# Optimization experiments

Measured on AMD Instinct MI355X. Metric: run time of the kernel, lower is better.

## Reference

```python
import jax, jax.numpy as jnp
import numpy as np

B, S, D, H, O, E, K = 4, 1024, 1024, 2048, 1024, 8, 2
LOAD_BALANCE_WEIGHT = 0.01


def setup_inputs() -> dict:
    key = jax.random.key(0)
    ks = jax.random.split(key, 9)
    scale = 0.02
    return {
        "x": jax.random.normal(ks[0], (B, S, D), jnp.float32),
        "Wg": scale * jax.random.normal(ks[1], (D, E), jnp.float32),
        "bg": jnp.zeros((E,), jnp.float32),
        "W1": scale * jax.random.normal(ks[2], (E, D, H), jnp.float32),
        "b1": jnp.zeros((E, H), jnp.float32),
        "W2": scale * jax.random.normal(ks[3], (E, H, H), jnp.float32),
        "b2": jnp.zeros((E, H), jnp.float32),
        "W3": scale * jax.random.normal(ks[4], (E, H, O), jnp.float32),
        "b3": jnp.zeros((E, O), jnp.float32),
    }


def reference(x, Wg, bg, W1, b1, W2, b2, W3, b3):
    # Eval-mode MoE: no gating noise, dropout is identity.
    b, s, d = x.shape
    e = Wg.shape[1]

    # --- gating: noisy top-k gating (noise off in eval) ---
    raw_gates = x @ Wg + bg                         # [B,S,E]
    topk_logits, topk_idx = jax.lax.top_k(raw_gates, K)  # [B,S,K]
    gates = jax.nn.softmax(topk_logits, axis=-1)    # [B,S,K]

    # Combine weights per expert: scatter top-k gates into [B,S,E].
    onehot = jax.nn.one_hot(topk_idx, e, dtype=x.dtype)      # [B,S,K,E]
    combine = jnp.sum(onehot * gates[..., None], axis=-2)    # [B,S,E]

    # --- expert MLPs (dense grouped GEMM over all tokens) ---
    xt = x.reshape(-1, d)            # [T,D]
    wt = combine.reshape(-1, e)      # [T,E]
    h = jax.nn.relu(jnp.einsum('td,edh->eth', xt, W1) + b1[:, None, :])
    h = jax.nn.relu(jnp.einsum('eth,ehg->etg', h, W2) + b2[:, None, :])
    y = jnp.einsum('eth,eho->eto', h, W3) + b3[:, None, :]   # [E,T,O]
    out = jnp.einsum('te,eto->to', wt, y).reshape(b, s, -1)  # [B,S,O]

    # --- auxiliary losses ---
    gate_probs = jax.nn.softmax(raw_gates, axis=-1)          # [B,S,E]
    avg_gate_probs = gate_probs.mean(axis=(0, 1))            # [E]
    avg_expert_counts = combine.mean(axis=(0, 1))            # [E]
    load_balance_loss = LOAD_BALANCE_WEIGHT * e * jnp.sum(avg_gate_probs * avg_expert_counts)
    gate_entropy = -jnp.sum(avg_gate_probs * jnp.log(avg_gate_probs + 1e-8))

    return out, load_balance_loss, avg_expert_counts, gate_entropy
```

## Files before the change

### kernel.cpp

```cpp
#include <hip/hip_runtime.h>
#include <hip/hip_bf16.h>
#include <math.h>

#define T_TOK 4096
#define D_IN  1024
#define H_DIM 2048
#define O_DIM 1024
#define NE    8
#define ROWCAP 9216
#define RT128  72

typedef __bf16 bf16x8 __attribute__((ext_vector_type(8)));
typedef __bf16 bf16x4 __attribute__((ext_vector_type(4)));
typedef float  f32x4  __attribute__((ext_vector_type(4)));

#define ELT(f, j) ((j) == 0 ? (f).x : (j) == 1 ? (f).y : (j) == 2 ? (f).z : (f).w)

__device__ __forceinline__ void gl_lds16(const void* g, void* l) {
    __builtin_amdgcn_global_load_lds(
        (const __attribute__((address_space(1))) void*)g,
        (__attribute__((address_space(3))) void*)l, 16, 0, 0);
}

__global__ __launch_bounds__(256) void gating_kernel(
    const float* __restrict__ x, const float* __restrict__ Wg, const float* __restrict__ bg,
    __bf16* __restrict__ xb, float* __restrict__ gates_tk, int* __restrict__ idx_tk,
    int* __restrict__ cnt_part, double* __restrict__ prob_part, double* __restrict__ gsum_part)
{
    __shared__ float WgS[8][1032];
    __shared__ float bgS[NE];
    __shared__ double tok_p[32][NE];
    __shared__ double tok_g[32][2];
    __shared__ int    tok_i[32][2];
    const int tid = threadIdx.x;

    for (int i = tid; i < D_IN * NE; i += 256)
        WgS[i >> 10][i & 1023] = Wg[i];
    if (tid < NE) bgS[tid] = bg[tid];

    {
        const size_t base = (size_t)blockIdx.x * 32 * D_IN;
        for (int i = tid * 4; i < 32 * D_IN; i += 256 * 4) {
            float4 v = *(const float4*)(x + base + i);
            bf16x4 b = {(__bf16)v.x, (__bf16)v.y, (__bf16)v.z, (__bf16)v.w};
            *(bf16x4*)(xb + base + i) = b;
        }
    }
    __syncthreads();

    const int tokL = tid >> 3;
    const int part = tid & 7;
    const int t = blockIdx.x * 32 + tokL;
    const float* xr = x + (size_t)t * D_IN + part * 128;

    double s[NE] = {0, 0, 0, 0, 0, 0, 0, 0};
    for (int j = 0; j < 128; j += 4) {
        float4 xv = *(const float4*)(xr + j);
        const float* w = &WgS[part][j * 8];
        #pragma unroll
        for (int jj = 0; jj < 4; ++jj) {
            double xd = (double)(ELT(xv, jj));
            #pragma unroll
            for (int e = 0; e < NE; ++e)
                s[e] += xd * (double)w[jj * 8 + e];
        }
    }
    #pragma unroll
    for (int off = 4; off; off >>= 1)
        #pragma unroll
        for (int e = 0; e < NE; ++e)
            s[e] += __shfl_xor(s[e], off);

    if (part == 0) {
        double rg[NE];
        #pragma unroll
        for (int e = 0; e < NE; ++e) rg[e] = s[e] + (double)bgS[e];
        int i0 = 0;
        #pragma unroll
        for (int e = 1; e < NE; ++e) if (rg[e] > rg[i0]) i0 = e;
        int i1 = -1;
        #pragma unroll
        for (int e = 0; e < NE; ++e) {
            if (e == i0) continue;
            if (i1 < 0 || rg[e] > rg[i1]) i1 = e;
        }
        double e1 = exp(rg[i1] - rg[i0]);
        double den = 1.0 + e1;
        gates_tk[t * 2] = (float)(1.0 / den); gates_tk[t * 2 + 1] = (float)(e1 / den);
        idx_tk[t * 2] = i0;   idx_tk[t * 2 + 1] = i1;
        tok_g[tokL][0] = 1.0 / den; tok_g[tokL][1] = e1 / den;
        tok_i[tokL][0] = i0;        tok_i[tokL][1] = i1;
        double mx = rg[0];
        #pragma unroll
        for (int e = 1; e < NE; ++e) mx = fmax(mx, rg[e]);
        double pe[NE], sum = 0.0;
        #pragma unroll
        for (int e = 0; e < NE; ++e) { pe[e] = exp(rg[e] - mx); sum += pe[e]; }
        #pragma unroll
        for (int e = 0; e < NE; ++e) tok_p[tokL][e] = pe[e] / sum;
    }
    __syncthreads();
    if (tid < NE) {
        double p = 0.0, g = 0.0; int c = 0;
        for (int i = 0; i < 32; ++i) {
            p += tok_p[i][tid];
            if (tok_i[i][0] == tid) { g += tok_g[i][0]; ++c; }
            if (tok_i[i][1] == tid) { g += tok_g[i][1]; ++c; }
        }
        prob_part[blockIdx.x * NE + tid] = p;
        gsum_part[blockIdx.x * NE + tid] = g;
        cnt_part[blockIdx.x * NE + tid] = c;
    }
}

__global__ __launch_bounds__(256) void route_tokens(
    const int* __restrict__ cnt_part, const int* __restrict__ idx_tk,
    int* __restrict__ poffset, int* __restrict__ totalp,
    int* __restrict__ token_ids, int* __restrict__ t2r)
{
    __shared__ int cntE[NE], baseE[NE];
    __shared__ int po[NE + 1];
    __shared__ int4 sb[256];
    const int tid = threadIdx.x;
    const int b = blockIdx.x;

    if (tid < NE) {
        int tot = 0, pre = 0;
        for (int g = 0; g < 128; ++g) {
            int v = cnt_part[g * NE + tid];
            tot += v;
            if (g < b * 8) pre += v;
        }
        cntE[tid] = tot;
        baseE[tid] = pre;
    }
    __syncthreads();
    if (tid == 0) {
        po[0] = 0;
        for (int e = 0; e < NE; ++e) po[e + 1] = po[e] + ((cntE[e] + 127) & ~127);
        if (b == 0) {
            for (int e = 0; e <= NE; ++e) poffset[e] = po[e];
            totalp[0] = po[NE];
        }
    }
    __syncthreads();

    const int t = b * 256 + tid;
    const int e0 = idx_tk[t * 2], e1 = idx_tk[t * 2 + 1];
    int4 p = {0, 0, 0, 0};
    ((int*)&p)[e0 >> 1] += 1 << ((e0 & 1) * 16);
    ((int*)&p)[e1 >> 1] += 1 << ((e1 & 1) * 16);
    sb[tid] = p;
    __syncthreads();
    for (int off = 1; off < 256; off <<= 1) {
        int4 v = sb[tid];
        int4 u = {0, 0, 0, 0};
        if (tid >= off) u = sb[tid - off];
        __syncthreads();
        v.x += u.x; v.y += u.y; v.z += u.z; v.w += u.w;
        sb[tid] = v;
        __syncthreads();
    }
    int4 inc = sb[tid];
    {
        int pos0 = ((((const int*)&inc)[e0 >> 1] >> ((e0 & 1) * 16)) & 0xffff) - 1;
        int r0 = po[e0] + baseE[e0] + pos0;
        token_ids[r0] = t; t2r[t * 2] = r0;
        int pos1 = ((((const int*)&inc)[e1 >> 1] >> ((e1 & 1) * 16)) & 0xffff) - 1;
        int r1 = po[e1] + baseE[e1] + pos1;
        token_ids[r1] = t; t2r[t * 2 + 1] = r1;
    }
    for (int e = 0; e < NE; ++e) {
        int c = cntE[e], base = po[e], pc = po[e + 1] - po[e];
        for (int i = c + b * 256 + tid; i < pc; i += 16 * 256) token_ids[base + i] = 0;
    }
}

template<bool GATHER, bool RELU, bool OUTBF16>
__global__ __launch_bounds__(256) void gemm_expert(
    const __bf16* __restrict__ A, int lda,
    const float* __restrict__ Bw, int Kdim, int N,
    const float* __restrict__ bias,
    void* __restrict__ Out, int ldo,
    const int* __restrict__ token_ids,
    const int* __restrict__ poffset,
    const int* __restrict__ totalp)
{
    __shared__ __bf16 As[128 * 64];
    __shared__ __bf16 Bs[128 * 64];
    const int tid = threadIdx.x;
    const int row0 = blockIdx.y * 128;
    if (row0 >= totalp[0]) return;
    int e = 0;
    while (e < NE - 1 && row0 >= poffset[e + 1]) ++e;
    const int n0 = blockIdx.x * 128;
    const float* Be = Bw + (size_t)e * Kdim * N;
    const float* biase = bias + (size_t)e * N;

    const int srow = tid >> 3;
    const int jperm = (tid & 7) ^ (srow & 7);
    const int scol = jperm * 8;
    int arow_g[4];
    #pragma unroll
    for (int c = 0; c < 4; ++c) {
        int r = row0 + c * 32 + srow;
        arow_g[c] = GATHER ? token_ids[r] : r;
    }

    const int rg = tid >> 5;
    const int cB = tid & 31;
    const float* bsrc0 = Be + (size_t)rg * 8 * N + n0 + cB * 4;

    const int lane = tid & 63;
    const int quad = lane >> 4;
    const int m16  = lane & 15;
    const int wave = tid >> 6;
    const int wm = wave >> 1, wn = wave & 1;

    f32x4 acc[4][4];
    #pragma unroll
    for (int i = 0; i < 4; ++i)
        #pragma unroll
        for (int j = 0; j < 4; ++j)
            acc[i][j] = (f32x4){0.f, 0.f, 0.f, 0.f};

    const int niter = Kdim >> 6;

    float4 r[8];
    #pragma unroll
    for (int i = 0; i < 8; ++i)
        r[i] = *(const float4*)(bsrc0 + (size_t)i * N);

    for (int kt = 0; kt < niter; ++kt) {
        const int kofs = kt * 64 + scol;
        #pragma unroll
        for (int c = 0; c < 4; ++c)
            gl_lds16(A + (size_t)arow_g[c] * lda + kofs, (char*)As + c * 4096 + tid * 16);
        #pragma unroll
        for (int j = 0; j < 4; ++j) {
            const int n = cB * 4 + j;
            const int key = (n & 7) ^ ((n >> 4) & 3);
            bf16x8 v;
            #pragma unroll
            for (int i = 0; i < 8; ++i) v[i] = (__bf16)(ELT(r[i], j));
            *(bf16x8*)&Bs[n * 64 + ((rg ^ key) << 3)] = v;
        }
        __syncthreads();
        if (kt + 1 < niter) {
            const float* bsrc = bsrc0 + (size_t)(kt + 1) * 64 * N;
            #pragma unroll
            for (int i = 0; i < 8; ++i)
                r[i] = *(const float4*)(bsrc + (size_t)i * N);
        }
        #pragma unroll
        for (int ks = 0; ks < 2; ++ks) {
            const int c0 = (ks << 2) | quad;
            const int pA = c0 ^ (m16 & 7);
            bf16x8 af[4], bfr[4];
            #pragma unroll
            for (int i = 0; i < 4; ++i)
                af[i] = *(const bf16x8*)&As[(wm * 64 + i * 16 + m16) * 64 + pA * 8];
            #pragma unroll
            for (int j = 0; j < 4; ++j) {
                const int pB = pA ^ j;
                bfr[j] = *(const bf16x8*)&Bs[(wn * 64 + j * 16 + m16) * 64 + pB * 8];
            }
            #pragma unroll
            for (int i = 0; i < 4; ++i)
                #pragma unroll
                for (int j = 0; j < 4; ++j)
                    acc[i][j] = __builtin_amdgcn_mfma_f32_16x16x32_bf16(af[i], bfr[j], acc[i][j], 0, 0, 0);
        }
        __syncthreads();
    }
    #pragma unroll
    for (int i = 0; i < 4; ++i)
        #pragma unroll
        for (int j = 0; j < 4; ++j)
            #pragma unroll
            for (int rr = 0; rr < 4; ++rr) {
                int grow = row0 + wm * 64 + i * 16 + quad * 4 + rr;
                int gcol = n0 + wn * 64 + j * 16 + m16;
                float v = acc[i][j][rr] + biase[gcol];
                if (RELU) v = v > 0.f ? v : 0.f;
                if (OUTBF16) ((__bf16*)Out)[(size_t)grow * ldo + gcol] = (__bf16)v;
                else         ((float*)Out)[(size_t)grow * ldo + gcol] = v;
            }
}

__global__ __launch_bounds__(256) void combine_out(
    const float* __restrict__ y, const float* __restrict__ gates_tk,
    const int* __restrict__ t2r, float* __restrict__ out,
    const double* __restrict__ prob_part, const double* __restrict__ gsum_part)
{
    const int t = blockIdx.x;
    const int o = threadIdx.x * 4;
    const int r0 = t2r[t * 2], r1 = t2r[t * 2 + 1];
    const float g0 = gates_tk[t * 2], g1 = gates_tk[t * 2 + 1];
    float4 a = *(const float4*)&y[(size_t)r0 * O_DIM + o];
    float4 b = *(const float4*)&y[(size_t)r1 * O_DIM + o];
    float4 c;
    c.x = g0 * a.x + g1 * b.x;
    c.y = g0 * a.y + g1 * b.y;
    c.z = g0 * a.z + g1 * b.z;
    c.w = g0 * a.w + g1 * b.w;
    *(float4*)&out[(size_t)t * O_DIM + o] = c;

    if (blockIdx.x == 0) {
        __shared__ double ps[NE], gs[NE];
        const int tid = threadIdx.x;
        if (tid < NE) {
            double p = 0.0, g = 0.0;
            for (int bb = 0; bb < 128; ++bb) {
                p += prob_part[bb * NE + tid];
                g += gsum_part[bb * NE + tid];
            }
            ps[tid] = p / (double)T_TOK;
            gs[tid] = g / (double)T_TOK;
            out[(size_t)T_TOK * O_DIM + 1 + tid] = (float)(g / (double)T_TOK);
        }
        __syncthreads();
        if (tid == 0) {
            double lb = 0.0, ent = 0.0;
            for (int e = 0; e < NE; ++e) {
                lb += ps[e] * gs[e];
                ent -= ps[e] * log(ps[e] + 1e-8);
            }
            out[(size_t)T_TOK * O_DIM] = (float)(0.01 * 8.0 * lb);
            out[(size_t)T_TOK * O_DIM + 9] = (float)ent;
        }
    }
}

extern "C" void kernel_launch(void* const* d_in, const int* in_sizes, int n_in,
                              void* d_out, int out_size, void* d_ws, size_t ws_size,
                              hipStream_t stream)
{
    const float* x  = (const float*)d_in[0];
    const float* Wg = (const float*)d_in[1];
    const float* bg = (const float*)d_in[2];
    const float* W1 = (const float*)d_in[3];
    const float* b1 = (const float*)d_in[4];
    const float* W2 = (const float*)d_in[5];
    const float* b2 = (const float*)d_in[6];
    const float* W3 = (const float*)d_in[7];
    const float* b3 = (const float*)d_in[8];
    float* out = (float*)d_out;
    char* ws = (char*)d_ws;

    size_t off = 0;
    __bf16* xb  = (__bf16*)(ws + off); off += (size_t)T_TOK * D_IN * 2;
    __bf16* h1  = (__bf16*)(ws + off);
    float*  y   = (float*) (ws + off); off += (size_t)ROWCAP * H_DIM * 2;
    __bf16* h2  = (__bf16*)(ws + off); off += (size_t)ROWCAP * H_DIM * 2;
    float* gates_tk = (float*)(ws + off); off += T_TOK * 2 * 4;
    int* idx_tk     = (int*)(ws + off);   off += T_TOK * 2 * 4;
    int* t2r        = (int*)(ws + off);   off += T_TOK * 2 * 4;
    int* token_ids  = (int*)(ws + off);   off += ROWCAP * 4;
    double* prob_part = (double*)(ws + off); off += 128 * NE * 8;
    double* gsum_part = (double*)(ws + off); off += 128 * NE * 8;
    int* cnt_part   = (int*)(ws + off);   off += 128 * NE * 4;
    int* poffset    = (int*)(ws + off);   off += (NE + 1) * 4;
    int* totalp     = (int*)(ws + off);   off += 16;

    gating_kernel<<<128, 256, 0, stream>>>(x, Wg, bg, xb, gates_tk, idx_tk,
                                           cnt_part, prob_part, gsum_part);
    route_tokens<<<16, 256, 0, stream>>>(cnt_part, idx_tk, poffset, totalp, token_ids, t2r);
    gemm_expert<true,  true,  true ><<<dim3(H_DIM / 128, RT128), 256, 0, stream>>>(
        xb, D_IN, W1, D_IN, H_DIM, b1, (void*)h1, H_DIM, token_ids, poffset, totalp);
    gemm_expert<false, true,  true ><<<dim3(H_DIM / 128, RT128), 256, 0, stream>>>(
        h1, H_DIM, W2, H_DIM, H_DIM, b2, (void*)h2, H_DIM, token_ids, poffset, totalp);
    gemm_expert<false, false, false><<<dim3(O_DIM / 128, RT128), 256, 0, stream>>>(
        h2, H_DIM, W3, H_DIM, O_DIM, b3, (void*)y, O_DIM, token_ids, poffset, totalp);
    combine_out<<<T_TOK, 256, 0, stream>>>(y, gates_tk, t2r, out, prob_part, gsum_part);
}
```

Before: 574.2 us.

## Fuse MoE pipeline into persistent megakernel with grid barriers and bf16 weight pre-conversion

Replaces the six separate launches with one persistent kernel of 512 blocks. Phases are separated by an atomic grid barrier, and GEMM tiles are spread across blocks in a strided loop. While the gating blocks run, the other blocks convert W1/W2/W3 from fp32 to bf16 in workspace, so the GEMMs load half-width weights and skip per-tile conversion. This trades launch gaps and repeated fp32 weight traffic for a full weight conversion pass every call and barrier overhead. It also relies on all 512 blocks being co-resident, and the barrier's bounded spin could silently break ordering.

Result: slower. 1.757 ms (+205.9%).

```diff
diff --git a/kernel.cpp b/kernel.cpp
--- a/kernel.cpp
+++ b/kernel.cpp
@@ -8,7 +8,8 @@
 #define O_DIM 1024
 #define NE    8
 #define ROWCAP 9216
-#define RT128  72
+#define NBLK  512
+#define GBLK  128
 
 typedef __bf16 bf16x8 __attribute__((ext_vector_type(8)));
 typedef __bf16 bf16x4 __attribute__((ext_vector_type(4)));
@@ -22,41 +23,82 @@
         (__attribute__((address_space(3))) void*)l, 16, 0, 0);
 }
 
-__global__ __launch_bounds__(256) void gating_kernel(
-    const float* __restrict__ x, const float* __restrict__ Wg, const float* __restrict__ bg,
-    __bf16* __restrict__ xb, float* __restrict__ gates_tk, int* __restrict__ idx_tk,
-    int* __restrict__ cnt_part, double* __restrict__ prob_part, double* __restrict__ gsum_part)
-{
-    __shared__ float WgS[8][1032];
-    __shared__ float bgS[NE];
-    __shared__ double tok_p[32][NE];
-    __shared__ double tok_g[32][2];
-    __shared__ int    tok_i[32][2];
-    const int tid = threadIdx.x;
-
+struct MoeArgs {
+    const float *x, *Wg, *bg, *W1, *b1, *W2, *b2, *W3, *b3;
+    float* out;
+    __bf16 *xb, *h1, *h2;
+    float* y;
+    __bf16 *W1b, *W2b, *W3b;
+    float* gates_tk;
+    int *idx_tk, *t2r, *token_ids;
+    double *prob_part, *gsum_part;
+    int *cnt_part, *poffset, *totalp;
+    int *bar;
+};
+
+__device__ __forceinline__ void grid_barrier(int* bar, int phase)
+{
+    __syncthreads();
+    __threadfence();
+    if (threadIdx.x == 0) {
+        __hip_atomic_fetch_add(bar, 1, __ATOMIC_RELEASE, __HIP_MEMORY_SCOPE_AGENT);
+        const int target = phase * NBLK;
+        int spins = 0;
+        while (__hip_atomic_load(bar, __ATOMIC_ACQUIRE, __HIP_MEMORY_SCOPE_AGENT) < target) {
+            __builtin_amdgcn_s_sleep(2);
+            if (++spins > (1 << 20)) break;
+        }
+    }
+    __syncthreads();
+    __threadfence();
+}
+
+union SharedU {
+    struct {
+        float WgS[8][1032];
+        float bgS[NE];
+        double tok_p[32][NE];
+        double tok_g[32][2];
+        int    tok_i[32][2];
+    } g;
+    struct {
+        int cntE[NE], baseE[NE], po[NE + 1];
+        int4 sb[256];
+    } r;
+    struct {
+        __bf16 As[128 * 64];
+        __bf16 Bs[128 * 64];
+    } m;
+    struct {
+        double ps[NE], gs[NE];
+    } f;
+};
+
+__device__ void gating_body(const int b, const int tid, const MoeArgs& a, SharedU& sh)
+{
     for (int i = tid; i < D_IN * NE; i += 256)
-        WgS[i >> 10][i & 1023] = Wg[i];
-    if (tid < NE) bgS[tid] = bg[tid];
+        sh.g.WgS[i >> 10][i & 1023] = a.Wg[i];
+    if (tid < NE) sh.g.bgS[tid] = a.bg[tid];
 
     {
-        const size_t base = (size_t)blockIdx.x * 32 * D_IN;
+        const size_t base = (size_t)b * 32 * D_IN;
         for (int i = tid * 4; i < 32 * D_IN; i += 256 * 4) {
-            float4 v = *(const float4*)(x + base + i);
-            bf16x4 b = {(__bf16)v.x, (__bf16)v.y, (__bf16)v.z, (__bf16)v.w};
-            *(bf16x4*)(xb + base + i) = b;
+            float4 v = *(const float4*)(a.x + base + i);
+            bf16x4 bv = {(__bf16)v.x, (__bf16)v.y, (__bf16)v.z, (__bf16)v.w};
+            *(bf16x4*)(a.xb + base + i) = bv;
         }
     }
     __syncthreads();
 
     const int tokL = tid >> 3;
     const int part = tid & 7;
-    const int t = blockIdx.x * 32 + tokL;
-    const float* xr = x + (size_t)t * D_IN + part * 128;
+    const int t = b * 32 + tokL;
+    const float* xr = a.x + (size_t)t * D_IN + part * 128;
 
     double s[NE] = {0, 0, 0, 0, 0, 0, 0, 0};
     for (int j = 0; j < 128; j += 4) {
         float4 xv = *(const float4*)(xr + j);
-        const float* w = &WgS[part][j * 8];
+        const float* w = &sh.g.WgS[part][j * 8];
         #pragma unroll
         for (int jj = 0; jj < 4; ++jj) {
             double xd = (double)(ELT(xv, jj));
@@ -74,7 +116,7 @@
     if (part == 0) {
         double rg[NE];
         #pragma unroll
-        for (int e = 0; e < NE; ++e) rg[e] = s[e] + (double)bgS[e];
+        for (int e = 0; e < NE; ++e) rg[e] = s[e] + (double)sh.g.bgS[e];
         int i0 = 0;
         #pragma unroll
         for (int e = 1; e < NE; ++e) if (rg[e] > rg[i0]) i0 = e;
@@ -86,10 +128,10 @@
         }
         double e1 = exp(rg[i1] - rg[i0]);
         double den = 1.0 + e1;
-        gates_tk[t * 2] = (float)(1.0 / den); gates_tk[t * 2 + 1] = (float)(e1 / den);
-        idx_tk[t * 2] = i0;   idx_tk[t * 2 + 1] = i1;
-        tok_g[tokL][0] = 1.0 / den; tok_g[tokL][1] = e1 / den;
-        tok_i[tokL][0] = i0;        tok_i[tokL][1] = i1;
+        a.gates_tk[t * 2] = (float)(1.0 / den); a.gates_tk[t * 2 + 1] = (float)(e1 / den);
+        a.idx_tk[t * 2] = i0;   a.idx_tk[t * 2 + 1] = i1;
+        sh.g.tok_g[tokL][0] = 1.0 / den; sh.g.tok_g[tokL][1] = e1 / den;
+        sh.g.tok_i[tokL][0] = i0;        sh.g.tok_i[tokL][1] = i1;
         double mx = rg[0];
         #pragma unroll
         for (int e = 1; e < NE; ++e) mx = fmax(mx, rg[e]);
@@ -97,37 +139,51 @@
         #pragma unroll
         for (int e = 0; e < NE; ++e) { pe[e] = exp(rg[e] - mx); sum += pe[e]; }
         #pragma unroll
-        for (int e = 0; e < NE; ++e) tok_p[tokL][e] = pe[e] / sum;
+        for (int e = 0; e < NE; ++e) sh.g.tok_p[tokL][e] = pe[e] / sum;
     }
     __syncthreads();
     if (tid < NE) {
         double p = 0.0, g = 0.0; int c = 0;
         for (int i = 0; i < 32; ++i) {
-            p += tok_p[i][tid];
-            if (tok_i[i][0] == tid) { g += tok_g[i][0]; ++c; }
-            if (tok_i[i][1] == tid) { g += tok_g[i][1]; ++c; }
-        }
-        prob_part[blockIdx.x * NE + tid] = p;
-        gsum_part[blockIdx.x * NE + tid] = g;
-        cnt_part[blockIdx.x * NE + tid] = c;
-    }
-}
-
-__global__ __launch_bounds__(256) void route_tokens(
-    const int* __restrict__ cnt_part, const int* __restrict__ idx_tk,
-    int* __restrict__ poffset, int* __restrict__ totalp,
-    int* __restrict__ token_ids, int* __restrict__ t2r)
-{
-    __shared__ int cntE[NE], baseE[NE];
-    __shared__ int po[NE + 1];
-    __shared__ int4 sb[256];
-    const int tid = threadIdx.x;
-    const int b = blockIdx.x;
+            p += sh.g.tok_p[i][tid];
+            if (sh.g.tok_i[i][0] == tid) { g += sh.g.tok_g[i][0]; ++c; }
+            if (sh.g.tok_i[i][1] == tid) { g += sh.g.tok_g[i][1]; ++c; }
+        }
+        a.prob_part[b * NE + tid] = p;
+        a.gsum_part[b * NE + tid] = g;
+        a.cnt_part[b * NE + tid] = c;
+    }
+}
+
+__device__ __forceinline__ void cvt_range(const float* __restrict__ src, __bf16* __restrict__ dst,
+                                          size_t n8, size_t start, size_t stride)
+{
+    for (size_t i = start; i < n8; i += stride) {
+        float4 va = ((const float4*)src)[2 * i];
+        float4 vb = ((const float4*)src)[2 * i + 1];
+        bf16x8 v = {(__bf16)va.x, (__bf16)va.y, (__bf16)va.z, (__bf16)va.w,
+                    (__bf16)vb.x, (__bf16)vb.y, (__bf16)vb.z, (__bf16)vb.w};
+        *(bf16x8*)(dst + i * 8) = v;
+    }
+}
+
+__device__ void cvt_body(const int cb, const int tid, const MoeArgs& a)
+{
+    const size_t start = (size_t)cb * 256 + tid;
+    const size_t stride = (size_t)(NBLK - GBLK) * 256;
+    cvt_range(a.W1, a.W1b, (size_t)NE * D_IN * H_DIM / 8, start, stride);
+    cvt_range(a.W2, a.W2b, (size_t)NE * H_DIM * H_DIM / 8, start, stride);
+    cvt_range(a.W3, a.W3b, (size_t)NE * H_DIM * O_DIM / 8, start, stride);
+}
+
+__device__ void route_body(const int b, const int tid, const MoeArgs& a, SharedU& sh)
+{
+    int* cntE = sh.r.cntE; int* baseE = sh.r.baseE; int* po = sh.r.po; int4* sb = sh.r.sb;
 
     if (tid < NE) {
         int tot = 0, pre = 0;
         for (int g = 0; g < 128; ++g) {
-            int v = cnt_part[g * NE + tid];
+            int v = a.cnt_part[g * NE + tid];
             tot += v;
             if (g < b * 8) pre += v;
         }
@@ -139,14 +195,14 @@
         po[0] = 0;
         for (int e = 0; e < NE; ++e) po[e + 1] = po[e] + ((cntE[e] + 127) & ~127);
         if (b == 0) {
-            for (int e = 0; e <= NE; ++e) poffset[e] = po[e];
-            totalp[0] = po[NE];
+            for (int e = 0; e <= NE; ++e) a.poffset[e] = po[e];
+            a.totalp[0] = po[NE];
         }
     }
     __syncthreads();
 
     const int t = b * 256 + tid;
-    const int e0 = idx_tk[t * 2], e1 = idx_tk[t * 2 + 1];
+    const int e0 = a.idx_tk[t * 2], e1 = a.idx_tk[t * 2 + 1];
     int4 p = {0, 0, 0, 0};
     ((int*)&p)[e0 >> 1] += 1 << ((e0 & 1) * 16);
     ((int*)&p)[e1 >> 1] += 1 << ((e1 & 1) * 16);
@@ -165,36 +221,32 @@
     {
         int pos0 = ((((const int*)&inc)[e0 >> 1] >> ((e0 & 1) * 16)) & 0xffff) - 1;
         int r0 = po[e0] + baseE[e0] + pos0;
-        token_ids[r0] = t; t2r[t * 2] = r0;
+        a.token_ids[r0] = t; a.t2r[t * 2] = r0;
         int pos1 = ((((const int*)&inc)[e1 >> 1] >> ((e1 & 1) * 16)) & 0xffff) - 1;
         int r1 = po[e1] + baseE[e1] + pos1;
-        token_ids[r1] = t; t2r[t * 2 + 1] = r1;
+        a.token_ids[r1] = t; a.t2r[t * 2 + 1] = r1;
     }
     for (int e = 0; e < NE; ++e) {
         int c = cntE[e], base = po[e], pc = po[e + 1] - po[e];
-        for (int i = c + b * 256 + tid; i < pc; i += 16 * 256) token_ids[base + i] = 0;
+        for (int i = c + b * 256 + tid; i < pc; i += 16 * 256) a.token_ids[base + i] = 0;
     }
 }
 
 template<bool GATHER, bool RELU, bool OUTBF16>
-__global__ __launch_bounds__(256) void gemm_expert(
+__device__ __forceinline__ void gemm_tile(
+    SharedU& sh, const int tid, const int n0, const int row0,
     const __bf16* __restrict__ A, int lda,
-    const float* __restrict__ Bw, int Kdim, int N,
+    const __bf16* __restrict__ Bw, int Kdim, int N,
     const float* __restrict__ bias,
     void* __restrict__ Out, int ldo,
     const int* __restrict__ token_ids,
-    const int* __restrict__ poffset,
-    const int* __restrict__ totalp)
-{
-    __shared__ __bf16 As[128 * 64];
-    __shared__ __bf16 Bs[128 * 64];
-    const int tid = threadIdx.x;
-    const int row0 = blockIdx.y * 128;
-    if (row0 >= totalp[0]) return;
+    const int* __restrict__ poffset)
+{
+    __bf16* As = sh.m.As;
+    __bf16* Bs = sh.m.Bs;
     int e = 0;
     while (e < NE - 1 && row0 >= poffset[e + 1]) ++e;
-    const int n0 = blockIdx.x * 128;
-    const float* Be = Bw + (size_t)e * Kdim * N;
+    const __bf16* Be = Bw + (size_t)e * Kdim * N;
     const float* biase = bias + (size_t)e * N;
 
     const int srow = tid >> 3;
@@ -209,7 +261,7 @@
 
     const int rg = tid >> 5;
     const int cB = tid & 31;
-    const float* bsrc0 = Be + (size_t)rg * 8 * N + n0 + cB * 4;
+    const __bf16* bsrc0 = Be + (size_t)rg * 8 * N + n0 + cB * 4;
 
     const int lane = tid & 63;
     const int quad = lane >> 4;
@@ -226,10 +278,10 @@
 
     const int niter = Kdim >> 6;
 
-    float4 r[8];
+    bf16x4 r[8];
     #pragma unroll
     for (int i = 0; i < 8; ++i)
-        r[i] = *(const float4*)(bsrc0 + (size_t)i * N);
+        r[i] = *(const bf16x4*)(bsrc0 + (size_t)i * N);
 
     for (int kt = 0; kt < niter; ++kt) {
         const int kofs = kt * 64 + scol;
@@ -242,15 +294,15 @@
             const int key = (n & 7) ^ ((n >> 4) & 3);
             bf16x8 v;
             #pragma unroll
-            for (int i = 0; i < 8; ++i) v[i] = (__bf16)(ELT(r[i], j));
+            for (int i = 0; i < 8; ++i) v[i] = r[i][j];
             *(bf16x8*)&Bs[n * 64 + ((rg ^ key) << 3)] = v;
         }
         __syncthreads();
         if (kt + 1 < niter) {
-            const float* bsrc = bsrc0 + (size_t)(kt + 1) * 64 * N;
+            const __bf16* bsrc = bsrc0 + (size_t)(kt + 1) * 64 * N;
             #pragma unroll
             for (int i = 0; i < 8; ++i)
-                r[i] = *(const float4*)(bsrc + (size_t)i * N);
+                r[i] = *(const bf16x4*)(bsrc + (size_t)i * N);
         }
         #pragma unroll
         for (int ks = 0; ks < 2; ++ks) {
@@ -288,71 +340,101 @@
             }
 }
 
-__global__ __launch_bounds__(256) void combine_out(
-    const float* __restrict__ y, const float* __restrict__ gates_tk,
-    const int* __restrict__ t2r, float* __restrict__ out,
-    const double* __restrict__ prob_part, const double* __restrict__ gsum_part)
-{
-    const int t = blockIdx.x;
-    const int o = threadIdx.x * 4;
-    const int r0 = t2r[t * 2], r1 = t2r[t * 2 + 1];
-    const float g0 = gates_tk[t * 2], g1 = gates_tk[t * 2 + 1];
-    float4 a = *(const float4*)&y[(size_t)r0 * O_DIM + o];
-    float4 b = *(const float4*)&y[(size_t)r1 * O_DIM + o];
-    float4 c;
-    c.x = g0 * a.x + g1 * b.x;
-    c.y = g0 * a.y + g1 * b.y;
-    c.z = g0 * a.z + g1 * b.z;
-    c.w = g0 * a.w + g1 * b.w;
-    *(float4*)&out[(size_t)t * O_DIM + o] = c;
-
-    if (blockIdx.x == 0) {
-        __shared__ double ps[NE], gs[NE];
-        const int tid = threadIdx.x;
+template<bool GATHER, bool RELU, bool OUTBF16>
+__device__ void gemm_phase(
+    SharedU& sh, const int bid, const int tid, const MoeArgs& a,
+    const __bf16* A, int lda, const __bf16* Bw, int Kdim, int N,
+    const float* bias, void* Out, int ldo)
+{
+    const int rtiles = (a.totalp[0] + 127) >> 7;
+    const int nx = N >> 7;
+    const int ntiles = nx * rtiles;
+    for (int tile = bid; tile < ntiles; tile += NBLK) {
+        const int n0 = (tile % nx) * 128;
+        const int row0 = (tile / nx) * 128;
+        gemm_tile<GATHER, RELU, OUTBF16>(sh, tid, n0, row0, A, lda, Bw, Kdim, N,
+                                         bias, Out, ldo, a.token_ids, a.poffset);
+    }
+}
+
+__device__ void combine_body(const int bid, const int tid, const MoeArgs& a, SharedU& sh)
+{
+    if (bid == 0) {
         if (tid < NE) {
             double p = 0.0, g = 0.0;
             for (int bb = 0; bb < 128; ++bb) {
-                p += prob_part[bb * NE + tid];
-                g += gsum_part[bb * NE + tid];
+                p += a.prob_part[bb * NE + tid];
+                g += a.gsum_part[bb * NE + tid];
             }
-            ps[tid] = p / (double)T_TOK;
-            gs[tid] = g / (double)T_TOK;
-            out[(size_t)T_TOK * O_DIM + 1 + tid] = (float)(g / (double)T_TOK);
+            sh.f.ps[tid] = p / (double)T_TOK;
+            sh.f.gs[tid] = g / (double)T_TOK;
+            a.out[(size_t)T_TOK * O_DIM + 1 + tid] = (float)(g / (double)T_TOK);
         }
         __syncthreads();
         if (tid == 0) {
             double lb = 0.0, ent = 0.0;
             for (int e = 0; e < NE; ++e) {
-                lb += ps[e] * gs[e];
-                ent -= ps[e] * log(ps[e] + 1e-8);
+                lb += sh.f.ps[e] * sh.f.gs[e];
+                ent -= sh.f.ps[e] * log(sh.f.ps[e] + 1e-8);
             }
-            out[(size_t)T_TOK * O_DIM] = (float)(0.01 * 8.0 * lb);
-            out[(size_t)T_TOK * O_DIM + 9] = (float)ent;
-        }
-    }
+            a.out[(size_t)T_TOK * O_DIM] = (float)(0.01 * 8.0 * lb);
+            a.out[(size_t)T_TOK * O_DIM + 9] = (float)ent;
+        }
+    }
+    const int o = tid * 4;
+    for (int t = bid; t < T_TOK; t += NBLK) {
+        const int r0 = a.t2r[t * 2], r1 = a.t2r[t * 2 + 1];
+        const float g0 = a.gates_tk[t * 2], g1 = a.gates_tk[t * 2 + 1];
+        float4 va = *(const float4*)&a.y[(size_t)r0 * O_DIM + o];
+        float4 vb = *(const float4*)&a.y[(size_t)r1 * O_DIM + o];
+        float4 c;
+        c.x = g0 * va.x + g1 * vb.x;
+        c.y = g0 * va.y + g1 * vb.y;
+        c.z = g0 * va.z + g1 * vb.z;
+        c.w = g0 * va.w + g1 * vb.w;
+        *(float4*)&a.out[(size_t)t * O_DIM + o] = c;
+    }
+}
+
+__global__ __launch_bounds__(256, 2) void moe_mega(MoeArgs a)
+{
+    __shared__ SharedU sh;
+    const int bid = blockIdx.x;
+    const int tid = threadIdx.x;
+
+    if (bid < GBLK) gating_body(bid, tid, a, sh);
+    else            cvt_body(bid - GBLK, tid, a);
+    grid_barrier(a.bar, 1);
+
+    if (bid < 16) route_body(bid, tid, a, sh);
+    grid_barrier(a.bar, 2);
+
+    gemm_phase<true,  true,  true >(sh, bid, tid, a, a.xb, D_IN, a.W1b, D_IN, H_DIM,
+                                    a.b1, (void*)a.h1, H_DIM);
+    grid_barrier(a.bar, 3);
+    gemm_phase<false, true,  true >(sh, bid, tid, a, a.h1, H_DIM, a.W2b, H_DIM, H_DIM,
+                                    a.b2, (void*)a.h2, H_DIM);
+    grid_barrier(a.bar, 4);
+    gemm_phase<false, false, false>(sh, bid, tid, a, a.h2, H_DIM, a.W3b, H_DIM, O_DIM,
+                                    a.b3, (void*)a.y, O_DIM);
+    grid_barrier(a.bar, 5);
+
+    combine_body(bid, tid, a, sh);
 }
 
 extern "C" void kernel_launch(void* const* d_in, const int* in_sizes, int n_in,
                               void* d_out, int out_size, void* d_ws, size_t ws_size,
                               hipStream_t stream)
 {
-    const float* x  = (const float*)d_in[0];
-    const float* Wg = (const float*)d_in[1];
-    const float* bg = (const float*)d_in[2];
-    const float* W1 = (const float*)d_in[3];
-    const float* b1 = (const float*)d_in[4];
-    const float* W2 = (const float*)d_in[5];
-    const float* b2 = (const float*)d_in[6];
-    const float* W3 = (const float*)d_in[7];
-    const float* b3 = (const float*)d_in[8];
-    float* out = (float*)d_out;
     char* ws = (char*)d_ws;
-
     size_t off = 0;
     __bf16* xb  = (__bf16*)(ws + off); off += (size_t)T_TOK * D_IN * 2;
     __bf16* h1  = (__bf16*)(ws + off);
     float*  y   = (float*) (ws + off); off += (size_t)ROWCAP * H_DIM * 2;
     __bf16* h2  = (__bf16*)(ws + off); off += (size_t)ROWCAP * H_DIM * 2;
+    __bf16* W1b = (__bf16*)(ws + off); off += (size_t)NE * D_IN * H_DIM * 2;
+    __bf16* W2b = (__bf16*)(ws + off); off += (size_t)NE * H_DIM * H_DIM * 2;
+    __bf16* W3b = (__bf16*)(ws + off); off += (size_t)NE * H_DIM * O_DIM * 2;
     float* gates_tk = (float*)(ws + off); off += T_TOK * 2 * 4;
     int* idx_tk     = (int*)(ws + off);   off += T_TOK * 2 * 4;
     int* t2r        = (int*)(ws + off);   off += T_TOK * 2 * 4;
@@ -362,15 +444,27 @@
     int* cnt_part   = (int*)(ws + off);   off += 128 * NE * 4;
     int* poffset    = (int*)(ws + off);   off += (NE + 1) * 4;
     int* totalp     = (int*)(ws + off);   off += 16;
-
-    gating_kernel<<<128, 256, 0, stream>>>(x, Wg, bg, xb, gates_tk, idx_tk,
-                                           cnt_part, prob_part, gsum_part);
-    route_tokens<<<16, 256, 0, stream>>>(cnt_part, idx_tk, poffset, totalp, token_ids, t2r);
-    gemm_expert<true,  true,  true ><<<dim3(H_DIM / 128, RT128), 256, 0, stream>>>(
-        xb, D_IN, W1, D_IN, H_DIM, b1, (void*)h1, H_DIM, token_ids, poffset, totalp);
-    gemm_expert<false, true,  true ><<<dim3(H_DIM / 128, RT128), 256, 0, stream>>>(
-        h1, H_DIM, W2, H_DIM, H_DIM, b2, (void*)h2, H_DIM, token_ids, poffset, totalp);
-    gemm_expert<false, false, false><<<dim3(O_DIM / 128, RT128), 256, 0, stream>>>(
-        h2, H_DIM, W3, H_DIM, O_DIM, b3, (void*)y, O_DIM, token_ids, poffset, totalp);
-    combine_out<<<T_TOK, 256, 0, stream>>>(y, gates_tk, t2r, out, prob_part, gsum_part);
-}
+    int* bar        = (int*)(ws + off);   off += 64;
+
+    hipMemsetAsync(bar, 0, 64, stream);
+
+    MoeArgs a;
+    a.x  = (const float*)d_in[0];
+    a.Wg = (const float*)d_in[1];
+    a.bg = (const float*)d_in[2];
+    a.W1 = (const float*)d_in[3];
+    a.b1 = (const float*)d_in[4];
+    a.W2 = (const float*)d_in[5];
+    a.b2 = (const float*)d_in[6];
+    a.W3 = (const float*)d_in[7];
+    a.b3 = (const float*)d_in[8];
+    a.out = (float*)d_out;
+    a.xb = xb; a.h1 = h1; a.h2 = h2; a.y = y;
+    a.W1b = W1b; a.W2b = W2b; a.W3b = W3b;
+    a.gates_tk = gates_tk; a.idx_tk = idx_tk; a.t2r = t2r; a.token_ids = token_ids;
+    a.prob_part = prob_part; a.gsum_part = gsum_part; a.cnt_part = cnt_part;
+    a.poffset = poffset; a.totalp = totalp;
+    a.bar = bar;
+
+    moe_mega<<<dim3(NBLK), dim3(256), 0, stream>>>(a);
+}
```
